# Kernel tuning notes

Measured on AMD Instinct MI355X. Metric: run time of the kernel, lower is better.

## Reference

```python
import jax, jax.numpy as jnp
import numpy as np

N_NODES = 100000
N_EDGES = 800000


def gcn_layer(x, W, b, src, dst, n):
    # PyG GCNConv (normalize=True): x @ W, add self-loops, sym-normalized mean aggregation, + bias
    h = x @ W  # [N, out]
    deg = jax.ops.segment_sum(jnp.ones_like(src, dtype=h.dtype), dst, num_segments=n)
    dinv = jnp.where(deg > 0, jax.lax.rsqrt(jnp.maximum(deg, 1.0)), 0.0)
    norm = dinv[src] * dinv[dst]  # [E+N]
    msg = h[src] * norm[:, None]  # gather + scale
    out = jax.ops.segment_sum(msg, dst, num_segments=n)  # scatter-add
    return out + b


def setup_inputs() -> dict:
    key = jax.random.key(0)
    k1, k2, k3, k4 = jax.random.split(key, 4)
    x = jax.random.normal(k1, (N_NODES, 128), dtype=jnp.float32)
    edge_index = jax.random.randint(k2, (2, N_EDGES), 0, N_NODES, dtype=jnp.int64)
    W1 = jax.random.normal(k3, (128, 64), dtype=jnp.float32) * (1.0 / np.sqrt(128))
    b1 = jnp.zeros((64,), dtype=jnp.float32)
    W2 = jax.random.normal(k4, (64, 40), dtype=jnp.float32) * (1.0 / np.sqrt(64))
    b2 = jnp.zeros((40,), dtype=jnp.float32)
    return {"x": x, "edge_index": edge_index, "W1": W1, "b1": b1, "W2": W2, "b2": b2}


def reference(x, edge_index, W1, b1, W2, b2):
    n = x.shape[0]
    loop = jnp.arange(n, dtype=edge_index.dtype)
    src = jnp.concatenate([edge_index[0], loop])  # add self-loops
    dst = jnp.concatenate([edge_index[1], loop])
    h = jax.nn.relu(gcn_layer(x, W1, b1, src, dst, n))
    # dropout is identity in eval mode (self.training=False)
    out = gcn_layer(h, W2, b2, src, dst, n)
    return jax.nn.log_softmax(out, axis=1)
```

## Files before the change

### kernel.cpp

```cpp
#include <hip/hip_runtime.h>
#include <hip/hip_fp16.h>
#include <math.h>


typedef _Float16 f16x8 __attribute__((ext_vector_type(8)));
typedef float    f32x4 __attribute__((ext_vector_type(4)));

__global__ void zero_kernel(int* __restrict__ p, int n) {
    int i = blockIdx.x * blockDim.x + threadIdx.x;
    if (i < n) p[i] = 0;
}

__global__ void deg_rank_kernel(const int* __restrict__ dst, int* __restrict__ degi,
                                int* __restrict__ rank, int E) {
    int i = blockIdx.x * blockDim.x + threadIdx.x;
    if (i < E) rank[i] = atomicAdd(&degi[dst[i]], 1);
}

__global__ __launch_bounds__(256) void blocksum_kernel(const int* __restrict__ degi,
                                                       int* __restrict__ partial, int n) {
    __shared__ int sm[256];
    int t = threadIdx.x;
    int base = blockIdx.x * 1024 + t * 4;
    int s = 0;
#pragma unroll
    for (int j = 0; j < 4; ++j) { int i = base + j; if (i < n) s += degi[i]; }
    sm[t] = s;
    __syncthreads();
    for (int off = 128; off > 0; off >>= 1) {
        if (t < off) sm[t] += sm[t + off];
        __syncthreads();
    }
    if (t == 0) partial[blockIdx.x] = sm[0];
}

__global__ __launch_bounds__(256) void offsets_kernel(int* __restrict__ degi,
                                                      const int* __restrict__ partial,
                                                      int* __restrict__ rowstart,
                                                      int n, int nb) {
    __shared__ int sm[256];
    __shared__ int pbase_s;
    int t = threadIdx.x;
    int pv = (t < nb) ? partial[t] : 0;
    sm[t] = pv;
    __syncthreads();
    for (int off = 1; off < 256; off <<= 1) {
        int x = (t >= off) ? sm[t - off] : 0;
        __syncthreads();
        sm[t] += x;
        __syncthreads();
    }
    if (t == 0) pbase_s = (blockIdx.x > 0) ? sm[blockIdx.x - 1] : 0;
    __syncthreads();
    int pbase = pbase_s;
    __syncthreads();

    int base = blockIdx.x * 1024 + t * 4;
    int v[4]; int s = 0;
#pragma unroll
    for (int j = 0; j < 4; ++j) { v[j] = (base + j < n) ? degi[base + j] : 0; s += v[j]; }
    sm[t] = s;
    __syncthreads();
    for (int off = 1; off < 256; off <<= 1) {
        int x = (t >= off) ? sm[t - off] : 0;
        __syncthreads();
        sm[t] += x;
        __syncthreads();
    }
    int run = pbase + (sm[t] - s);
#pragma unroll
    for (int j = 0; j < 4; ++j) {
        if (base + j < n) {
            rowstart[base + j] = run; run += v[j];
            ((float*)degi)[base + j] = rsqrtf((float)v[j] + 1.0f);
        }
    }
}

__global__ void fill_kernel(const int* __restrict__ src, const int* __restrict__ dst,
                            const int* __restrict__ rank, const float* __restrict__ dinv,
                            const int* __restrict__ rowstart, int2* __restrict__ csr, int E) {
    int e = blockIdx.x * blockDim.x + threadIdx.x;
    if (e >= E) return;
    int s = src[e], t = dst[e];
    float nrm = dinv[s] * dinv[t];
    unsigned short us = __half_as_ushort(__float2half_rn(nrm));
    int packed = (int)(((unsigned)us << 16) | us);
    int pos = rowstart[t] + rank[e];
    csr[pos] = make_int2(s, packed);
}

__global__ __launch_bounds__(256) void gemm1_mfma(const float* __restrict__ X,
                                                  const float* __restrict__ W,
                                                  _Float16* __restrict__ H, int n) {
    __shared__ _Float16 Ws[64 * 128];
    int t = threadIdx.x;
    int rowbase = blockIdx.x * 64;

    for (int i = t; i < 2048; i += 256) {
        int k = i >> 4;
        int nn0 = (i & 15) * 4;
        float4 v = *reinterpret_cast<const float4*>(W + (size_t)k * 64 + nn0);
        const float* vp = reinterpret_cast<const float*>(&v);
#pragma unroll
        for (int j = 0; j < 4; ++j) {
            int nn = nn0 + j;
            Ws[nn * 128 + (k ^ ((nn & 7) << 3))] = (_Float16)vp[j];
        }
    }

    int w = t >> 6;
    int l = t & 63;
    int lr = l & 15;
    int lk = l >> 4;
    int arow = rowbase + 16 * w + lr;
    int ar = arow < n ? arow : n - 1;

    f16x8 a[4];
#pragma unroll
    for (int kc = 0; kc < 4; ++kc) {
        const float* xp = X + (size_t)ar * 128 + kc * 32 + lk * 8;
        float4 v0 = *reinterpret_cast<const float4*>(xp);
        float4 v1 = *reinterpret_cast<const float4*>(xp + 4);
        f16x8 hv = { (_Float16)v0.x, (_Float16)v0.y, (_Float16)v0.z, (_Float16)v0.w,
                     (_Float16)v1.x, (_Float16)v1.y, (_Float16)v1.z, (_Float16)v1.w };
        a[kc] = hv;
    }
    __syncthreads();

    f32x4 acc[4] = {};
#pragma unroll
    for (int nt = 0; nt < 4; ++nt) {
        int nrow = 16 * nt + lr;
#pragma unroll
        for (int kc = 0; kc < 4; ++kc) {
            int k8 = kc * 32 + lk * 8;
            f16x8 b = *reinterpret_cast<f16x8*>(&Ws[nrow * 128 + (k8 ^ ((nrow & 7) << 3))]);
            acc[nt] = __builtin_amdgcn_mfma_f32_16x16x32_f16(a[kc], b, acc[nt], 0, 0, 0);
        }
    }
#pragma unroll
    for (int nt = 0; nt < 4; ++nt) {
#pragma unroll
        for (int r = 0; r < 4; ++r) {
            int grow = rowbase + 16 * w + lk * 4 + r;
            if (grow < n) H[(size_t)grow * 64 + nt * 16 + lr] = (_Float16)acc[nt][r];
        }
    }
}

static __device__ __forceinline__ __half2 relu_h2(__half2 v) {
    unsigned u = *reinterpret_cast<unsigned*>(&v);
    unsigned neg = (u >> 15) & 0x00010001u;
    u &= ~(neg * 0xFFFFu);
    return *reinterpret_cast<__half2*>(&u);
}

template <bool RELU, bool BIAS>
__global__ __launch_bounds__(256) void gather64h_kernel(const __half* __restrict__ Hh,
                                                        const int2* __restrict__ csr,
                                                        const int* __restrict__ rowstart,
                                                        const float* __restrict__ dinv,
                                                        const float* __restrict__ b,
                                                        __half* __restrict__ Oh, int n, int E) {
    int gt = blockIdx.x * blockDim.x + threadIdx.x;
    int node = gt >> 3;
    if (node >= n) return;
    int fl = gt & 7;
    const float4* H4 = reinterpret_cast<const float4*>(Hh);
    int rs = rowstart[node];
    int re = (node + 1 < n) ? rowstart[node + 1] : E;
    __half2 acc[4];
#pragma unroll
    for (int q = 0; q < 4; ++q) acc[q] = __float2half2_rn(0.0f);

    int e = rs;
    while (__any(e < re)) {
        int srcrow[4]; __half2 nh[4]; float4 raw[4];
#pragma unroll
        for (int u = 0; u < 4; ++u) {
            int ee = e + u;
            bool valid = ee < re;
            int2 c = csr[valid ? ee : rs];
            srcrow[u] = valid ? c.x : 0;
            int ni = valid ? c.y : 0;
            nh[u] = *reinterpret_cast<__half2*>(&ni);
        }
#pragma unroll
        for (int u = 0; u < 4; ++u)
            raw[u] = H4[srcrow[u] * 8 + fl];
#pragma unroll
        for (int u = 0; u < 4; ++u) {
            const __half2* hp = reinterpret_cast<const __half2*>(&raw[u]);
#pragma unroll
            for (int q = 0; q < 4; ++q)
                acc[q] = __hfma2(hp[q], nh[u], acc[q]);
        }
        e += 4;
    }
    {
        float di = dinv[node];
        __half2 d2 = __float2half2_rn(di * di);
        float4 raw = H4[node * 8 + fl];
        const __half2* hp = reinterpret_cast<const __half2*>(&raw);
#pragma unroll
        for (int q = 0; q < 4; ++q) acc[q] = __hfma2(hp[q], d2, acc[q]);
    }
    if (BIAS) {
        float4 b0 = reinterpret_cast<const float4*>(b)[fl * 2];
        float4 b1 = reinterpret_cast<const float4*>(b)[fl * 2 + 1];
        acc[0] = __hadd2(acc[0], __float22half2_rn(make_float2(b0.x, b0.y)));
        acc[1] = __hadd2(acc[1], __float22half2_rn(make_float2(b0.z, b0.w)));
        acc[2] = __hadd2(acc[2], __float22half2_rn(make_float2(b1.x, b1.y)));
        acc[3] = __hadd2(acc[3], __float22half2_rn(make_float2(b1.z, b1.w)));
    }
    if (RELU) {
#pragma unroll
        for (int q = 0; q < 4; ++q) acc[q] = relu_h2(acc[q]);
    }
    float4 o;
    __half2* op = reinterpret_cast<__half2*>(&o);
#pragma unroll
    for (int q = 0; q < 4; ++q) op[q] = acc[q];
    *reinterpret_cast<float4*>(Oh + (size_t)node * 64 + fl * 8) = o;
}

__global__ __launch_bounds__(256) void gather_gemm2_softmax(
        const __half* __restrict__ Hh, const int2* __restrict__ csr,
        const int* __restrict__ rowstart, const float* __restrict__ dinv,
        const float* __restrict__ W, const float* __restrict__ b,
        float* __restrict__ out, int n, int E) {
    constexpr int BM = 64, K = 64, C = 40, XP = 68, HP = 41;
    __shared__ float Xs[BM * XP];
    __shared__ float Ws[K * C];
    __shared__ float bs[C];
    __shared__ float rowm[BM], rowls[BM];
    int t = threadIdx.x;
    int rowbase = blockIdx.x * BM;

    for (int i = t; i < K * C / 4; i += 256)
        ((float4*)Ws)[i] = ((const float4*)W)[i];
    if (t < C) bs[t] = b[t];

    int team = t >> 3, fl = t & 7;
    const float4* H4 = reinterpret_cast<const float4*>(Hh);
#pragma unroll
    for (int pass = 0; pass < 2; ++pass) {
        int lrow = team + pass * 32;
        int node = rowbase + lrow;
        __half2 acc[4];
#pragma unroll
        for (int q = 0; q < 4; ++q) acc[q] = __float2half2_rn(0.0f);
        if (node < n) {
            int rs = rowstart[node];
            int re = (node + 1 < n) ? rowstart[node + 1] : E;
            int e = rs;
            while (__any(e < re)) {
                int srcrow[4]; __half2 nh[4]; float4 raw[4];
#pragma unroll
                for (int u = 0; u < 4; ++u) {
                    int ee = e + u;
                    bool valid = ee < re;
                    int2 c = csr[valid ? ee : rs];
                    srcrow[u] = valid ? c.x : 0;
                    int ni = valid ? c.y : 0;
                    nh[u] = *reinterpret_cast<__half2*>(&ni);
                }
#pragma unroll
                for (int u = 0; u < 4; ++u)
                    raw[u] = H4[srcrow[u] * 8 + fl];
#pragma unroll
                for (int u = 0; u < 4; ++u) {
                    const __half2* hp = reinterpret_cast<const __half2*>(&raw[u]);
#pragma unroll
                    for (int q = 0; q < 4; ++q)
                        acc[q] = __hfma2(hp[q], nh[u], acc[q]);
                }
                e += 4;
            }
            float di = dinv[node];
            __half2 d2 = __float2half2_rn(di * di);
            float4 raw = H4[node * 8 + fl];
            const __half2* hp = reinterpret_cast<const __half2*>(&raw);
#pragma unroll
            for (int q = 0; q < 4; ++q) acc[q] = __hfma2(hp[q], d2, acc[q]);
        }
        float* dp = &Xs[lrow * XP + fl * 8];
        float2 f0 = __half22float2(acc[0]), f1 = __half22float2(acc[1]);
        float2 f2 = __half22float2(acc[2]), f3 = __half22float2(acc[3]);
        *reinterpret_cast<float4*>(dp)     = make_float4(f0.x, f0.y, f1.x, f1.y);
        *reinterpret_cast<float4*>(dp + 4) = make_float4(f2.x, f2.y, f3.x, f3.y);
    }
    __syncthreads();

    int tx = t % (C / 4);
    int ty = t / (C / 4);
    bool active = ty < BM / 4;
    float acc[4][4] = {};
    if (active) {
#pragma unroll
        for (int k0 = 0; k0 < K; k0 += 4) {
            float4 xq[4], wq[4];
#pragma unroll
            for (int i = 0; i < 4; ++i)
                xq[i] = *reinterpret_cast<const float4*>(&Xs[(ty * 4 + i) * XP + k0]);
#pragma unroll
            for (int j = 0; j < 4; ++j)
                wq[j] = *reinterpret_cast<const float4*>(&Ws[(k0 + j) * C + tx * 4]);
#pragma unroll
            for (int i = 0; i < 4; ++i) {
                const float* xa = reinterpret_cast<const float*>(&xq[i]);
#pragma unroll
                for (int j = 0; j < 4; ++j) {
                    const float* wb = reinterpret_cast<const float*>(&wq[j]);
                    acc[i][0] += xa[j] * wb[0];
                    acc[i][1] += xa[j] * wb[1];
                    acc[i][2] += xa[j] * wb[2];
                    acc[i][3] += xa[j] * wb[3];
                }
            }
        }
    }
    __syncthreads();
    float* Hs = Xs;
    if (active) {
#pragma unroll
        for (int i = 0; i < 4; ++i) {
            int r = ty * 4 + i;
#pragma unroll
            for (int j = 0; j < 4; ++j)
                Hs[r * HP + tx * 4 + j] = acc[i][j] + bs[tx * 4 + j];
        }
    }
    __syncthreads();
    if (t < BM) {
        float m = -INFINITY;
        for (int j = 0; j < C; ++j) m = fmaxf(m, Hs[t * HP + j]);
        float s = 0.f;
        for (int j = 0; j < C; ++j) s += __expf(Hs[t * HP + j] - m);
        rowm[t] = m; rowls[t] = __logf(s);
    }
    __syncthreads();
    for (int idx = t; idx < BM * C; idx += 256) {
        int r = idx / C, c = idx - r * C;
        int gr = rowbase + r;
        if (gr < n) out[(size_t)gr * C + c] = Hs[r * HP + c] - rowm[r] - rowls[r];
    }
}

extern "C" void kernel_launch(void* const* d_in, const int* in_sizes, int n_in,
                              void* d_out, int out_size, void* d_ws, size_t ws_size,
                              hipStream_t stream) {
    const float* x  = (const float*)d_in[0];
    const int*   ei = (const int*)d_in[1];
    const float* W1 = (const float*)d_in[2];
    const float* b1 = (const float*)d_in[3];
    const float* W2 = (const float*)d_in[4];
    const float* b2 = (const float*)d_in[5];
    float* out = (float*)d_out;

    const int n = in_sizes[0] / 128;
    const int E = in_sizes[1] / 2;
    const int* src = ei;
    const int* dst = ei + E;

    auto al = [](size_t x) { return (x + 255) & ~(size_t)255; };
    float* ws = (float*)d_ws;
    size_t o_deg  = 0;
    size_t o_cnt  = al(n);
    size_t o_part = o_cnt + al(n);
    size_t o_rank = o_part + 1024;
    size_t o_csr  = o_rank + al(E);
    size_t o_h1   = o_csr + al((size_t)2 * E);
    size_t o_out1 = o_h1 + al((size_t)n * 32);

    int*    degi     = (int*)(ws + o_deg);
    float*  dinv     = (float*)(ws + o_deg);
    int*    rowstart = (int*)(ws + o_cnt);
    int*    partial  = (int*)(ws + o_part);
    int*    rank     = (int*)(ws + o_rank);
    int2*   csr      = (int2*)(ws + o_csr);
    __half* h1       = (__half*)(ws + o_h1);
    __half* out1     = (__half*)(ws + o_out1);

    const int NB = (n + 1023) / 1024;

    zero_kernel<<<(n + 255) / 256, 256, 0, stream>>>(degi, n);
    deg_rank_kernel<<<(E + 255) / 256, 256, 0, stream>>>(dst, degi, rank, E);
    blocksum_kernel<<<NB, 256, 0, stream>>>(degi, partial, n);
    offsets_kernel<<<NB, 256, 0, stream>>>(degi, partial, rowstart, n, NB);
    fill_kernel<<<(E + 255) / 256, 256, 0, stream>>>(src, dst, rank, dinv, rowstart, csr, E);

    gemm1_mfma<<<(n + 63) / 64, 256, 0, stream>>>(x, W1, (_Float16*)h1, n);
    gather64h_kernel<true, true><<<((size_t)n * 8 + 255) / 256, 256, 0, stream>>>(
        h1, csr, rowstart, dinv, b1, out1, n, E);
    gather_gemm2_softmax<<<(n + 63) / 64, 256, 0, stream>>>(
        out1, csr, rowstart, dinv, W2, b2, out, n, E);
}
```

Baseline: 137.4 us.

## Co-schedule GEMM1 tiles with degree-count and CSR-fill kernels

Splits the first-layer GEMM tiles into two halves and runs them in the same launches as the degree/rank atomic kernel and the CSR fill kernel, using block-index ranges to pick the role. This removes one launch and lets the latency-bound atomic and scatter work overlap with the compute-heavy GEMM. In exchange, every block in those kernels reserves the 16 KB shared tile even on the atomic and fill paths, which may reduce occupancy for those blocks.

Result: no change. 135.6 us (-1.4%).

```diff
diff --git a/kernel.cpp b/kernel.cpp
--- a/kernel.cpp
+++ b/kernel.cpp
@@ -11,10 +11,99 @@
     if (i < n) p[i] = 0;
 }
 
-__global__ void deg_rank_kernel(const int* __restrict__ dst, int* __restrict__ degi,
-                                int* __restrict__ rank, int E) {
-    int i = blockIdx.x * blockDim.x + threadIdx.x;
-    if (i < E) rank[i] = atomicAdd(&degi[dst[i]], 1);
+static __device__ __forceinline__ void gemm1_tile(const float* __restrict__ X,
+                                                  const float* __restrict__ W,
+                                                  _Float16* __restrict__ H, int n,
+                                                  int tile, _Float16* Ws ) {
+    int t = threadIdx.x;
+    int rowbase = tile * 64;
+
+    for (int i = t; i < 2048; i += 256) {
+        int k = i >> 4;
+        int nn0 = (i & 15) * 4;
+        float4 v = *reinterpret_cast<const float4*>(W + (size_t)k * 64 + nn0);
+        const float* vp = reinterpret_cast<const float*>(&v);
+#pragma unroll
+        for (int j = 0; j < 4; ++j) {
+            int nn = nn0 + j;
+            Ws[nn * 128 + (k ^ ((nn & 7) << 3))] = (_Float16)vp[j];
+        }
+    }
+
+    int w = t >> 6;
+    int l = t & 63;
+    int lr = l & 15;
+    int lk = l >> 4;
+    int arow = rowbase + 16 * w + lr;
+    int ar = arow < n ? arow : n - 1;
+
+    f16x8 a[4];
+#pragma unroll
+    for (int kc = 0; kc < 4; ++kc) {
+        const float* xp = X + (size_t)ar * 128 + kc * 32 + lk * 8;
+        float4 v0 = *reinterpret_cast<const float4*>(xp);
+        float4 v1 = *reinterpret_cast<const float4*>(xp + 4);
+        f16x8 hv = { (_Float16)v0.x, (_Float16)v0.y, (_Float16)v0.z, (_Float16)v0.w,
+                     (_Float16)v1.x, (_Float16)v1.y, (_Float16)v1.z, (_Float16)v1.w };
+        a[kc] = hv;
+    }
+    __syncthreads();
+
+    f32x4 acc[4] = {};
+#pragma unroll
+    for (int nt = 0; nt < 4; ++nt) {
+        int nrow = 16 * nt + lr;
+#pragma unroll
+        for (int kc = 0; kc < 4; ++kc) {
+            int k8 = kc * 32 + lk * 8;
+            f16x8 b = *reinterpret_cast<f16x8*>(&Ws[nrow * 128 + (k8 ^ ((nrow & 7) << 3))]);
+            acc[nt] = __builtin_amdgcn_mfma_f32_16x16x32_f16(a[kc], b, acc[nt], 0, 0, 0);
+        }
+    }
+#pragma unroll
+    for (int nt = 0; nt < 4; ++nt) {
+#pragma unroll
+        for (int r = 0; r < 4; ++r) {
+            int grow = rowbase + 16 * w + lk * 4 + r;
+            if (grow < n) H[(size_t)grow * 64 + nt * 16 + lr] = (_Float16)acc[nt][r];
+        }
+    }
+}
+
+__global__ __launch_bounds__(256) void degrank_gemm1_kernel(
+        const int* __restrict__ dst, int* __restrict__ degi, int* __restrict__ rank, int E,
+        const float* __restrict__ X, const float* __restrict__ W,
+        _Float16* __restrict__ H, int n, int nDeg) {
+    __shared__ _Float16 Ws[64 * 128];
+    int b = blockIdx.x;
+    if (b < nDeg) {
+        int i = b * 256 + threadIdx.x;
+        if (i < E) rank[i] = atomicAdd(&degi[dst[i]], 1);
+    } else {
+        gemm1_tile(X, W, H, n, b - nDeg, Ws);
+    }
+}
+
+__global__ __launch_bounds__(256) void fill_gemm1_kernel(
+        const int* __restrict__ src, const int* __restrict__ dst,
+        const int* __restrict__ rank, const float* __restrict__ dinv,
+        const int* __restrict__ rowstart, int2* __restrict__ csr, int E,
+        const float* __restrict__ X, const float* __restrict__ W,
+        _Float16* __restrict__ H, int n, int nFill, int tileOff) {
+    __shared__ _Float16 Ws[64 * 128];
+    int b = blockIdx.x;
+    if (b < nFill) {
+        int e = b * 256 + threadIdx.x;
+        if (e >= E) return;
+        int s = src[e], t = dst[e];
+        float nrm = dinv[s] * dinv[t];
+        unsigned short us = __half_as_ushort(__float2half_rn(nrm));
+        int packed = (int)(((unsigned)us << 16) | us);
+        int pos = rowstart[t] + rank[e];
+        csr[pos] = make_int2(s, packed);
+    } else {
+        gemm1_tile(X, W, H, n, b - nFill + tileOff, Ws);
+    }
 }
 
 __global__ __launch_bounds__(256) void blocksum_kernel(const int* __restrict__ degi,
@@ -73,78 +162,6 @@
         if (base + j < n) {
             rowstart[base + j] = run; run += v[j];
             ((float*)degi)[base + j] = rsqrtf((float)v[j] + 1.0f);
-        }
-    }
-}
-
-__global__ void fill_kernel(const int* __restrict__ src, const int* __restrict__ dst,
-                            const int* __restrict__ rank, const float* __restrict__ dinv,
-                            const int* __restrict__ rowstart, int2* __restrict__ csr, int E) {
-    int e = blockIdx.x * blockDim.x + threadIdx.x;
-    if (e >= E) return;
-    int s = src[e], t = dst[e];
-    float nrm = dinv[s] * dinv[t];
-    unsigned short us = __half_as_ushort(__float2half_rn(nrm));
-    int packed = (int)(((unsigned)us << 16) | us);
-    int pos = rowstart[t] + rank[e];
-    csr[pos] = make_int2(s, packed);
-}
-
-__global__ __launch_bounds__(256) void gemm1_mfma(const float* __restrict__ X,
-                                                  const float* __restrict__ W,
-                                                  _Float16* __restrict__ H, int n) {
-    __shared__ _Float16 Ws[64 * 128];
-    int t = threadIdx.x;
-    int rowbase = blockIdx.x * 64;
-
-    for (int i = t; i < 2048; i += 256) {
-        int k = i >> 4;
-        int nn0 = (i & 15) * 4;
-        float4 v = *reinterpret_cast<const float4*>(W + (size_t)k * 64 + nn0);
-        const float* vp = reinterpret_cast<const float*>(&v);
-#pragma unroll
-        for (int j = 0; j < 4; ++j) {
-            int nn = nn0 + j;
-            Ws[nn * 128 + (k ^ ((nn & 7) << 3))] = (_Float16)vp[j];
-        }
-    }
-
-    int w = t >> 6;
-    int l = t & 63;
-    int lr = l & 15;
-    int lk = l >> 4;
-    int arow = rowbase + 16 * w + lr;
-    int ar = arow < n ? arow : n - 1;
-
-    f16x8 a[4];
-#pragma unroll
-    for (int kc = 0; kc < 4; ++kc) {
-        const float* xp = X + (size_t)ar * 128 + kc * 32 + lk * 8;
-        float4 v0 = *reinterpret_cast<const float4*>(xp);
-        float4 v1 = *reinterpret_cast<const float4*>(xp + 4);
-        f16x8 hv = { (_Float16)v0.x, (_Float16)v0.y, (_Float16)v0.z, (_Float16)v0.w,
-                     (_Float16)v1.x, (_Float16)v1.y, (_Float16)v1.z, (_Float16)v1.w };
-        a[kc] = hv;
-    }
-    __syncthreads();
-
-    f32x4 acc[4] = {};
-#pragma unroll
-    for (int nt = 0; nt < 4; ++nt) {
-        int nrow = 16 * nt + lr;
-#pragma unroll
-        for (int kc = 0; kc < 4; ++kc) {
-            int k8 = kc * 32 + lk * 8;
-            f16x8 b = *reinterpret_cast<f16x8*>(&Ws[nrow * 128 + (k8 ^ ((nrow & 7) << 3))]);
-            acc[nt] = __builtin_amdgcn_mfma_f32_16x16x32_f16(a[kc], b, acc[nt], 0, 0, 0);
-        }
-    }
-#pragma unroll
-    for (int nt = 0; nt < 4; ++nt) {
-#pragma unroll
-        for (int r = 0; r < 4; ++r) {
-            int grow = rowbase + 16 * w + lk * 4 + r;
-            if (grow < n) H[(size_t)grow * 64 + nt * 16 + lr] = (_Float16)acc[nt][r];
         }
     }
 }
@@ -384,14 +401,18 @@
     __half* out1     = (__half*)(ws + o_out1);
 
     const int NB = (n + 1023) / 1024;
+    const int nDeg   = (E + 255) / 256;
+    const int ntiles = (n + 63) / 64;
+    const int tilesA = ntiles / 2;
+    const int tilesB = ntiles - tilesA;
 
     zero_kernel<<<(n + 255) / 256, 256, 0, stream>>>(degi, n);
-    deg_rank_kernel<<<(E + 255) / 256, 256, 0, stream>>>(dst, degi, rank, E);
+    degrank_gemm1_kernel<<<nDeg + tilesA, 256, 0, stream>>>(
+        dst, degi, rank, E, x, W1, (_Float16*)h1, n, nDeg);
     blocksum_kernel<<<NB, 256, 0, stream>>>(degi, partial, n);
     offsets_kernel<<<NB, 256, 0, stream>>>(degi, partial, rowstart, n, NB);
-    fill_kernel<<<(E + 255) / 256, 256, 0, stream>>>(src, dst, rank, dinv, rowstart, csr, E);
-
-    gemm1_mfma<<<(n + 63) / 64, 256, 0, stream>>>(x, W1, (_Float16*)h1, n);
+    fill_gemm1_kernel<<<nDeg + tilesB, 256, 0, stream>>>(
+        src, dst, rank, dinv, rowstart, csr, E, x, W1, (_Float16*)h1, n, nDeg, tilesA);
     gather64h_kernel<true, true><<<((size_t)n * 8 + 255) / 256, 256, 0, stream>>>(
         h1, csr, rowstart, dinv, b1, out1, n, E);
     gather_gemm2_softmax<<<(n + 63) / 64, 256, 0, stream>>>(
```
